# Optimization experiments

Measured on AMD Instinct MI355X. Metric: run time of the kernel, lower is better.

Reference implementation:

```python
import jax, jax.numpy as jnp
import numpy as np

# --- constants matching the torch module's default-camera / material / light setup ---
IMAGE_SIZE = 128
SCALE = 1.0
FOCAL = 12.0
R_MAT = jnp.array([[-1.0, 0.0, 0.0], [0.0, 1.0, 0.0], [0.0, 0.0, -1.0]], dtype=jnp.float32)
T_VEC = jnp.array([0.0, 0.0, 2.0 * SCALE], dtype=jnp.float32)
CAM_POS = jnp.array([0.0, 0.0, 2.0 * SCALE], dtype=jnp.float32)  # camera center in world coords
LIGHT_LOC = jnp.array([0.0, 1.0, 3.0], dtype=jnp.float32)
AMB_L, DIFF_L, SPEC_L = 0.5, 0.3, 0.2          # PointLights defaults
MAT_AMB, MAT_DIFF, MAT_SPEC = 1.0, 1.0, 0.6    # Materials(specular_color=0.6)
SHININESS = 10.0
TEXEL = jnp.array([142.0, 179.0, 247.0], dtype=jnp.float32) / 255.0  # uniform vertex color
BG = 1.0  # BlendParams background
EPS = 1e-8


def _normalize(v):
    return v / (jnp.linalg.norm(v, axis=-1, keepdims=True) + EPS)


def _render_one(verts, faces):
    """verts: [V,3] world space; faces: [F,3] int. Returns ([3,H,W] rgb*255, [1,H,W] alpha)."""
    H = W = IMAGE_SIZE
    # world -> view (PyTorch3D row-vector convention: x_view = x @ R + T)
    view = verts @ R_MAT + T_VEC              # [V,3]
    z = view[:, 2]                            # [V] view-space depth (>0 in front)
    ndc = FOCAL * view[:, :2] / z[:, None]    # [V,2] perspective projection to NDC
    tri = ndc[faces]                          # [F,3,2]
    tz = z[faces]                             # [F,3]

    # pixel centers in NDC (PyTorch3D: +x left, +y up)
    xs = 1.0 - (2.0 * jnp.arange(W) + 1.0) / W
    ys = 1.0 - (2.0 * jnp.arange(H) + 1.0) / H
    gy, gx = jnp.meshgrid(ys, xs, indexing='ij')
    px = gx.reshape(-1).astype(jnp.float32)   # [P]
    py = gy.reshape(-1).astype(jnp.float32)   # [P]

    v0, v1, v2 = tri[:, 0], tri[:, 1], tri[:, 2]   # [F,2]

    def edge(a, b):  # signed area cross(b-a, p-a) for all pixels -> [P,F]
        return ((b[:, 0] - a[:, 0])[None] * (py[:, None] - a[:, 1][None])
                - (b[:, 1] - a[:, 1])[None] * (px[:, None] - a[:, 0][None]))

    area = ((v1[:, 0] - v0[:, 0]) * (v2[:, 1] - v0[:, 1])
            - (v1[:, 1] - v0[:, 1]) * (v2[:, 0] - v0[:, 0]))   # [F]
    area_safe = jnp.where(jnp.abs(area) < EPS, EPS, area)
    b0 = edge(v1, v2) / area_safe             # [P,F]
    b1 = edge(v2, v0) / area_safe
    b2 = 1.0 - b0 - b1
    inside = (b0 >= 0) & (b1 >= 0) & (b2 >= 0) & (jnp.abs(area) > EPS)[None]

    # perspective-correct interpolated depth: z_pix = 1 / sum_i(b_i / z_i)
    S = b0 / tz[:, 0] + b1 / tz[:, 1] + b2 / tz[:, 2]
    depth = jnp.where(inside & (S > EPS), 1.0 / jnp.maximum(S, EPS), jnp.inf)
    fidx = jnp.argmin(depth, axis=1)          # [P] z-buffer winner (faces_per_pixel=1)
    hit = jnp.isfinite(jnp.min(depth, axis=1))

    # --- recompute barycentrics only for the winning face per pixel (cheap, [P]) ---
    f = faces[fidx]                           # [P,3]
    tv = ndc[f]                               # [P,3,2]
    tzp = z[f]                                # [P,3]
    a0, a1, a2 = tv[:, 0], tv[:, 1], tv[:, 2]

    def edge_p(a, b):
        return (b[:, 0] - a[:, 0]) * (py - a[:, 1]) - (b[:, 1] - a[:, 1]) * (px - a[:, 0])

    ar = (a1[:, 0] - a0[:, 0]) * (a2[:, 1] - a0[:, 1]) - (a1[:, 1] - a0[:, 1]) * (a2[:, 0] - a0[:, 0])
    ar = jnp.where(jnp.abs(ar) < EPS, EPS, ar)
    bb0 = edge_p(a1, a2) / ar
    bb1 = edge_p(a2, a0) / ar
    bb2 = 1.0 - bb0 - bb1
    w = jnp.stack([bb0 / tzp[:, 0], bb1 / tzp[:, 1], bb2 / tzp[:, 2]], axis=-1)
    pc = w / (jnp.sum(w, axis=-1, keepdims=True) + EPS)   # [P,3] perspective-correct barycentrics

    # --- vertex normals (world space) ---
    fv = verts[faces]                         # [F,3,3]
    fn = jnp.cross(fv[:, 1] - fv[:, 0], fv[:, 2] - fv[:, 0])  # [F,3]
    vn = (jnp.zeros_like(verts)
          .at[faces[:, 0]].add(fn)
          .at[faces[:, 1]].add(fn)
          .at[faces[:, 2]].add(fn))
    vn = _normalize(vn)

    # --- interpolate position/normal, Phong shade ---
    pos = jnp.einsum('pk,pkd->pd', pc, verts[f])   # [P,3]
    nrm = _normalize(jnp.einsum('pk,pkd->pd', pc, vn[f]))
    l = _normalize(LIGHT_LOC - pos)
    vdir = _normalize(CAM_POS - pos)
    ndl = jax.nn.relu(jnp.sum(nrm * l, axis=-1))          # [P]
    refl = 2.0 * jnp.sum(nrm * l, axis=-1, keepdims=True) * nrm - l
    spec_cos = jax.nn.relu(jnp.sum(refl * vdir, axis=-1))
    ambient = AMB_L * MAT_AMB
    diffuse = DIFF_L * MAT_DIFF * ndl
    specular = SPEC_L * MAT_SPEC * spec_cos ** SHININESS
    color = TEXEL[None] * (ambient + diffuse[:, None]) + specular[:, None]

    rgb = jnp.where(hit[:, None], color, BG)              # hard blend with white bg
    alpha = hit.astype(verts.dtype)
    img = rgb.reshape(H, W, 3).transpose(2, 0, 1) * 255.0  # [3,H,W]
    a = alpha.reshape(1, H, W)
    return img, a


def setup_inputs() -> dict:
    key = jax.random.key(0)
    k1, k2 = jax.random.split(key)
    B, V, F = 2, 1300, 2500
    vertices = jax.random.normal(k1, (B, V, 3), dtype=jnp.float32) * 0.05  # head-scale mesh near origin
    faces = jax.random.randint(k2, (F, 3), 0, V, dtype=jnp.int32)
    return {"vertices": vertices, "faces": faces}


def reference(vertices, faces):
    # ori_size == image_size, so the area-interpolation in the torch module is the identity.
    images, alphas = jax.lax.map(lambda v: _render_one(v, faces), vertices)
    return images, alphas
```

## Files before the change

kernel.cpp:

```cpp
#include <hip/hip_runtime.h>
#include <math.h>

#pragma clang fp contract(off)

#define IMG_H 128
#define IMG_W 128
#define HW (IMG_H * IMG_W)
#define NB 2
#define NV 1300
#define NF 2500
#define EPSF 1e-8f
#define NCHUNK 32
#define CHUNK ((NF + NCHUNK - 1) / NCHUNK)
#define NBLK (64 * NB * NCHUNK)

#define OFF_VN 41600
#define OFF_FACE 72800
#define OFF_DBUF 392800

#define DINIT 0x7F800000FFFFFFFFull

__global__ __launch_bounds__(256) void k_init(const float* __restrict__ verts,
                                              float4* __restrict__ vert,
                                              float* __restrict__ vn) {
    int i = blockIdx.x * 256 + threadIdx.x;
    if (i < NB * NV * 3) vn[i] = 0.0f;
    if (i < NB * NV) {
        float vx = verts[i * 3 + 0];
        float vy = verts[i * 3 + 1];
        float vz = verts[i * 3 + 2];
        float viewx = -vx;
        float viewy = vy;
        float z = 2.0f - vz;
        float ndcx = (12.0f * viewx) / z;
        float ndcy = (12.0f * viewy) / z;
        vert[i] = make_float4(ndcx, ndcy, z, 0.0f);
    }
}

__global__ __launch_bounds__(256) void k_face(const float* __restrict__ verts,
                                              const int* __restrict__ faces,
                                              const float4* __restrict__ vert,
                                              float* __restrict__ vn,
                                              float4* __restrict__ face) {
    int i = blockIdx.x * 256 + threadIdx.x;
    if (i >= NB * NF) return;
    int b = i / NF;
    int f = i - b * NF;
    int i0 = faces[f * 3 + 0];
    int i1 = faces[f * 3 + 1];
    int i2 = faces[f * 3 + 2];
    float4 p0 = vert[b * NV + i0];
    float4 p1 = vert[b * NV + i1];
    float4 p2 = vert[b * NV + i2];
    float t1 = (p1.x - p0.x) * (p2.y - p0.y);
    float t2 = (p1.y - p0.y) * (p2.x - p0.x);
    float area = t1 - t2;
    float aabs = fabsf(area);
    float area_safe = (aabs < EPSF) ? EPSF : area;
    bool valid = aabs > EPSF;
    float minx, maxx, miny, maxy;
    if (valid) {
        minx = fminf(p0.x, fminf(p1.x, p2.x)) - 1e-3f;
        maxx = fmaxf(p0.x, fmaxf(p1.x, p2.x)) + 1e-3f;
        miny = fminf(p0.y, fminf(p1.y, p2.y)) - 1e-3f;
        maxy = fmaxf(p0.y, fmaxf(p1.y, p2.y)) + 1e-3f;
    } else {
        minx = 1e30f; maxx = -1e30f; miny = 1e30f; maxy = -1e30f;
    }
    int o = (b * NF + f) * 4;
    face[o + 0] = make_float4(p2.x - p1.x, p2.y - p1.y, p1.x, p1.y);
    face[o + 1] = make_float4(p0.x - p2.x, p0.y - p2.y, p2.x, p2.y);
    face[o + 2] = make_float4(area_safe, p0.z, p1.z, p2.z);
    face[o + 3] = make_float4(minx, maxx, miny, maxy);

    const float* wv = verts + (size_t)b * NV * 3;
    float ax = wv[i1 * 3 + 0] - wv[i0 * 3 + 0];
    float ay = wv[i1 * 3 + 1] - wv[i0 * 3 + 1];
    float az = wv[i1 * 3 + 2] - wv[i0 * 3 + 2];
    float bx = wv[i2 * 3 + 0] - wv[i0 * 3 + 0];
    float by = wv[i2 * 3 + 1] - wv[i0 * 3 + 1];
    float bz = wv[i2 * 3 + 2] - wv[i0 * 3 + 2];
    float fnx = ay * bz - az * by;
    float fny = az * bx - ax * bz;
    float fnz = ax * by - ay * bx;
    float* vnb = vn + (size_t)b * NV * 3;
    atomicAdd(&vnb[i0 * 3 + 0], fnx);
    atomicAdd(&vnb[i0 * 3 + 1], fny);
    atomicAdd(&vnb[i0 * 3 + 2], fnz);
    atomicAdd(&vnb[i1 * 3 + 0], fnx);
    atomicAdd(&vnb[i1 * 3 + 1], fny);
    atomicAdd(&vnb[i1 * 3 + 2], fnz);
    atomicAdd(&vnb[i2 * 3 + 0], fnx);
    atomicAdd(&vnb[i2 * 3 + 1], fny);
    atomicAdd(&vnb[i2 * 3 + 2], fnz);
}

__global__ __launch_bounds__(256) void k_raster(const float4* __restrict__ face,
                                                unsigned long long* __restrict__ dbuf) {
    __shared__ float4 sface[CHUNK * 4];
    __shared__ int sidx[CHUNK];
    __shared__ int swbase[4];
    __shared__ int scnt;

    int idx = (blockIdx.x * 1213) & (NBLK - 1);
    int chunk = idx & (NCHUNK - 1);
    int tmp = idx >> 5;
    int b = tmp & 1;
    int tile = tmp >> 1;
    int f0 = chunk * CHUNK;
    int nf = NF - f0; if (nf > CHUNK) nf = CHUNK;

    int r0 = (tile >> 3) * 16;
    int c0 = (tile & 7) * 16;
    float txmax = 1.0f - (2.0f * (float)c0 + 1.0f) / 128.0f;
    float txmin = 1.0f - (2.0f * (float)(c0 + 15) + 1.0f) / 128.0f;
    float tymax = 1.0f - (2.0f * (float)r0 + 1.0f) / 128.0f;
    float tymin = 1.0f - (2.0f * (float)(r0 + 15) + 1.0f) / 128.0f;

    const float4* fb = face + (size_t)b * NF * 4;
    int t = threadIdx.x;
    int wid = t >> 6, lid = t & 63;
    bool pass = false;
    float4 bb;
    if (t < nf) {
        bb = fb[(f0 + t) * 4 + 3];
        pass = (bb.y >= txmin) && (bb.x <= txmax) && (bb.w >= tymin) && (bb.z <= tymax);
    }
    unsigned long long m = __ballot(pass);
    if (lid == 0) swbase[wid] = __popcll(m);
    __syncthreads();
    if (t == 0) {
        int acc = 0;
        for (int i2 = 0; i2 < 4; ++i2) { int cc = swbase[i2]; swbase[i2] = acc; acc += cc; }
        scnt = acc;
    }
    __syncthreads();
    if (pass) {
        int pos = swbase[wid] + __popcll(m & ((1ull << lid) - 1ull));
        sface[pos * 4 + 0] = fb[(f0 + t) * 4 + 0];
        sface[pos * 4 + 1] = fb[(f0 + t) * 4 + 1];
        sface[pos * 4 + 2] = fb[(f0 + t) * 4 + 2];
        sface[pos * 4 + 3] = bb;
        sidx[pos] = f0 + t;
    }
    __syncthreads();
    int cnt = scnt;

    int r = r0 + ((wid >> 1) * 8) + (lid >> 3);
    int c = c0 + ((wid & 1) * 8) + (lid & 7);
    int p = r * IMG_W + c;
    float px = 1.0f - (2.0f * (float)c + 1.0f) / 128.0f;
    float py = 1.0f - (2.0f * (float)r + 1.0f) / 128.0f;

    unsigned long long best = DINIT;
    for (int j = 0; j < cnt; ++j) {
        float4 fbb = sface[j * 4 + 3];
        if (px >= fbb.x && px <= fbb.y && py >= fbb.z && py <= fbb.w) {
            float4 E0 = sface[j * 4 + 0];
            float4 E1 = sface[j * 4 + 1];
            float4 FD = sface[j * 4 + 2];
            float u1 = E0.x * (py - E0.w);
            float u2 = E0.y * (px - E0.z);
            float e0 = u1 - u2;
            float u3 = E1.x * (py - E1.w);
            float u4 = E1.y * (px - E1.z);
            float e1 = u3 - u4;
            float as = FD.x;
            bool ok = (as > 0.0f) ? (e0 >= 0.0f && e1 >= 0.0f)
                                  : (e0 <= 0.0f && e1 <= 0.0f);
            if (ok) {
                float b0 = e0 / as;
                float b1 = e1 / as;
                float b2 = (1.0f - b0) - b1;
                if (b2 >= 0.0f) {
                    float S = ((b0 / FD.y) + (b1 / FD.z)) + (b2 / FD.w);
                    if (S > EPSF) {
                        float depth = 1.0f / fmaxf(S, EPSF);
                        unsigned long long pk =
                            ((unsigned long long)__float_as_uint(depth) << 32) |
                            (unsigned)sidx[j];
                        if (pk < best) best = pk;
                    }
                }
            }
        }
    }
    dbuf[((size_t)chunk * NB + b) * HW + p] = best;
}

__global__ __launch_bounds__(256) void k_shade(const float* __restrict__ verts,
                                               const int* __restrict__ faces,
                                               const float4* __restrict__ vert,
                                               const float* __restrict__ vn,
                                               const unsigned long long* __restrict__ dbuf,
                                               float* __restrict__ out) {
    int i = blockIdx.x * 256 + threadIdx.x;
    int b = i >> 14;
    int p = i & (HW - 1);
    unsigned long long pk = DINIT;
    for (int k = 0; k < NCHUNK; ++k) {
        unsigned long long v = dbuf[((size_t)k * NB + b) * HW + p];
        if (v < pk) pk = v;
    }
    unsigned dbits = (unsigned)(pk >> 32);
    bool hit = dbits < 0x7F800000u;
    float cr = 255.0f, cg = 255.0f, cb = 255.0f, alpha = 0.0f;
    if (hit) {
        alpha = 1.0f;
        int f = (int)(unsigned)(pk & 0xFFFFFFFFull);
        int row = p >> 7;
        int col = p & 127;
        float px = 1.0f - (2.0f * (float)col + 1.0f) / 128.0f;
        float py = 1.0f - (2.0f * (float)row + 1.0f) / 128.0f;
        int i0 = faces[f * 3 + 0];
        int i1 = faces[f * 3 + 1];
        int i2 = faces[f * 3 + 2];
        float4 a0 = vert[b * NV + i0];
        float4 a1 = vert[b * NV + i1];
        float4 a2 = vert[b * NV + i2];
        float t1 = (a1.x - a0.x) * (a2.y - a0.y);
        float t2 = (a1.y - a0.y) * (a2.x - a0.x);
        float ar = t1 - t2;
        ar = (fabsf(ar) < EPSF) ? EPSF : ar;
        float u1 = (a2.x - a1.x) * (py - a1.y);
        float u2 = (a2.y - a1.y) * (px - a1.x);
        float bb0 = (u1 - u2) / ar;
        float u3 = (a0.x - a2.x) * (py - a2.y);
        float u4 = (a0.y - a2.y) * (px - a2.x);
        float bb1 = (u3 - u4) / ar;
        float bb2 = (1.0f - bb0) - bb1;
        float w0 = bb0 / a0.z;
        float w1 = bb1 / a1.z;
        float w2 = bb2 / a2.z;
        float denom = ((w0 + w1) + w2) + EPSF;
        float pc0 = w0 / denom;
        float pc1 = w1 / denom;
        float pc2 = w2 / denom;

        const float* wv = verts + (size_t)b * NV * 3;
        float v0x = wv[i0 * 3 + 0], v0y = wv[i0 * 3 + 1], v0z = wv[i0 * 3 + 2];
        float v1x = wv[i1 * 3 + 0], v1y = wv[i1 * 3 + 1], v1z = wv[i1 * 3 + 2];
        float v2x = wv[i2 * 3 + 0], v2y = wv[i2 * 3 + 1], v2z = wv[i2 * 3 + 2];
        float posx = (pc0 * v0x + pc1 * v1x) + pc2 * v2x;
        float posy = (pc0 * v0y + pc1 * v1y) + pc2 * v2y;
        float posz = (pc0 * v0z + pc1 * v1z) + pc2 * v2z;

        const float* vnb = vn + (size_t)b * NV * 3;
        float n0x = vnb[i0 * 3 + 0], n0y = vnb[i0 * 3 + 1], n0z = vnb[i0 * 3 + 2];
        float n1x = vnb[i1 * 3 + 0], n1y = vnb[i1 * 3 + 1], n1z = vnb[i1 * 3 + 2];
        float n2x = vnb[i2 * 3 + 0], n2y = vnb[i2 * 3 + 1], n2z = vnb[i2 * 3 + 2];
        float in0 = 1.0f / (sqrtf(n0x * n0x + n0y * n0y + n0z * n0z) + EPSF);
        float in1 = 1.0f / (sqrtf(n1x * n1x + n1y * n1y + n1z * n1z) + EPSF);
        float in2 = 1.0f / (sqrtf(n2x * n2x + n2y * n2y + n2z * n2z) + EPSF);
        n0x *= in0; n0y *= in0; n0z *= in0;
        n1x *= in1; n1y *= in1; n1z *= in1;
        n2x *= in2; n2y *= in2; n2z *= in2;
        float nx = (pc0 * n0x + pc1 * n1x) + pc2 * n2x;
        float ny = (pc0 * n0y + pc1 * n1y) + pc2 * n2y;
        float nz = (pc0 * n0z + pc1 * n1z) + pc2 * n2z;
        float inn = 1.0f / (sqrtf(nx * nx + ny * ny + nz * nz) + EPSF);
        nx *= inn; ny *= inn; nz *= inn;

        float lx = 0.0f - posx, ly = 1.0f - posy, lz = 3.0f - posz;
        float iln = 1.0f / (sqrtf(lx * lx + ly * ly + lz * lz) + EPSF);
        lx *= iln; ly *= iln; lz *= iln;
        float vx = 0.0f - posx, vy = 0.0f - posy, vz = 2.0f - posz;
        float ivn = 1.0f / (sqrtf(vx * vx + vy * vy + vz * vz) + EPSF);
        vx *= ivn; vy *= ivn; vz *= ivn;

        float ndl = nx * lx + ny * ly + nz * lz;
        float ndlr = fmaxf(ndl, 0.0f);
        float rx = 2.0f * ndl * nx - lx;
        float ry = 2.0f * ndl * ny - ly;
        float rz = 2.0f * ndl * nz - lz;
        float sc = fmaxf(rx * vx + ry * vy + rz * vz, 0.0f);
        float spec = 0.2f * 0.6f * powf(sc, 10.0f);
        float shade = 0.5f * 1.0f + 0.3f * 1.0f * ndlr;
        cr = ((142.0f / 255.0f) * shade + spec) * 255.0f;
        cg = ((179.0f / 255.0f) * shade + spec) * 255.0f;
        cb = ((247.0f / 255.0f) * shade + spec) * 255.0f;
    }
    float* img = out + (size_t)b * 3 * HW;
    img[0 * HW + p] = cr;
    img[1 * HW + p] = cg;
    img[2 * HW + p] = cb;
    out[(size_t)NB * 3 * HW + (size_t)b * HW + p] = alpha;
}

extern "C" void kernel_launch(void* const* d_in, const int* in_sizes, int n_in,
                              void* d_out, int out_size, void* d_ws, size_t ws_size,
                              hipStream_t stream) {
    const float* verts = (const float*)d_in[0];
    const int* faces = (const int*)d_in[1];
    char* ws = (char*)d_ws;
    float4* vert = (float4*)(ws + 0);
    float* vn = (float*)(ws + OFF_VN);
    float4* face = (float4*)(ws + OFF_FACE);
    unsigned long long* dbuf = (unsigned long long*)(ws + OFF_DBUF);
    float* out = (float*)d_out;

    k_init<<<(NB * NV * 3 + 255) / 256, 256, 0, stream>>>(verts, vert, vn);
    k_face<<<(NB * NF + 255) / 256, 256, 0, stream>>>(verts, faces, vert, vn, face);
    k_raster<<<NBLK, 256, 0, stream>>>(face, dbuf);
    k_shade<<<(NB * HW) / 256, 256, 0, stream>>>(verts, faces, vert, vn, dbuf, out);
}
```

Baseline: 111.3 us.

## Fold vertex projection into face and shade kernels, shrink raster tiles to 128 threads

Removes the k_init kernel: the face and shade kernels now project vertices themselves, and the normal buffer is cleared with hipMemsetAsync. This saves a launch and the intermediate vertex buffer. The raster kernel switches to 128-thread blocks covering 8x16 tiles, which doubles the block count and drops one barrier from the compaction step. It also drops the blockIdx scrambling. The cost is some redundant projection arithmetic and less face reuse per block.

```diff
diff --git a/kernel.cpp b/kernel.cpp
--- a/kernel.cpp
+++ b/kernel.cpp
@@ -12,35 +12,16 @@
 #define EPSF 1e-8f
 #define NCHUNK 32
 #define CHUNK ((NF + NCHUNK - 1) / NCHUNK)
-#define NBLK (64 * NB * NCHUNK)
-
-#define OFF_VN 41600
-#define OFF_FACE 72800
-#define OFF_DBUF 392800
+#define NREG 128
+#define NBLK (NREG * NB * NCHUNK)
+
+#define OFF_FACE 31232
+#define OFF_DBUF 351488
 
 #define DINIT 0x7F800000FFFFFFFFull
-
-__global__ __launch_bounds__(256) void k_init(const float* __restrict__ verts,
-                                              float4* __restrict__ vert,
-                                              float* __restrict__ vn) {
-    int i = blockIdx.x * 256 + threadIdx.x;
-    if (i < NB * NV * 3) vn[i] = 0.0f;
-    if (i < NB * NV) {
-        float vx = verts[i * 3 + 0];
-        float vy = verts[i * 3 + 1];
-        float vz = verts[i * 3 + 2];
-        float viewx = -vx;
-        float viewy = vy;
-        float z = 2.0f - vz;
-        float ndcx = (12.0f * viewx) / z;
-        float ndcy = (12.0f * viewy) / z;
-        vert[i] = make_float4(ndcx, ndcy, z, 0.0f);
-    }
-}
 
 __global__ __launch_bounds__(256) void k_face(const float* __restrict__ verts,
                                               const int* __restrict__ faces,
-                                              const float4* __restrict__ vert,
                                               float* __restrict__ vn,
                                               float4* __restrict__ face) {
     int i = blockIdx.x * 256 + threadIdx.x;
@@ -50,37 +31,38 @@
     int i0 = faces[f * 3 + 0];
     int i1 = faces[f * 3 + 1];
     int i2 = faces[f * 3 + 2];
-    float4 p0 = vert[b * NV + i0];
-    float4 p1 = vert[b * NV + i1];
-    float4 p2 = vert[b * NV + i2];
-    float t1 = (p1.x - p0.x) * (p2.y - p0.y);
-    float t2 = (p1.y - p0.y) * (p2.x - p0.x);
+    const float* wv = verts + (size_t)b * NV * 3;
+    float v0x = wv[i0 * 3 + 0], v0y = wv[i0 * 3 + 1], v0z = wv[i0 * 3 + 2];
+    float v1x = wv[i1 * 3 + 0], v1y = wv[i1 * 3 + 1], v1z = wv[i1 * 3 + 2];
+    float v2x = wv[i2 * 3 + 0], v2y = wv[i2 * 3 + 1], v2z = wv[i2 * 3 + 2];
+    float z0 = 2.0f - v0z, z1 = 2.0f - v1z, z2 = 2.0f - v2z;
+    float p0x = (12.0f * (-v0x)) / z0, p0y = (12.0f * v0y) / z0;
+    float p1x = (12.0f * (-v1x)) / z1, p1y = (12.0f * v1y) / z1;
+    float p2x = (12.0f * (-v2x)) / z2, p2y = (12.0f * v2y) / z2;
+
+    float t1 = (p1x - p0x) * (p2y - p0y);
+    float t2 = (p1y - p0y) * (p2x - p0x);
     float area = t1 - t2;
     float aabs = fabsf(area);
     float area_safe = (aabs < EPSF) ? EPSF : area;
     bool valid = aabs > EPSF;
     float minx, maxx, miny, maxy;
     if (valid) {
-        minx = fminf(p0.x, fminf(p1.x, p2.x)) - 1e-3f;
-        maxx = fmaxf(p0.x, fmaxf(p1.x, p2.x)) + 1e-3f;
-        miny = fminf(p0.y, fminf(p1.y, p2.y)) - 1e-3f;
-        maxy = fmaxf(p0.y, fmaxf(p1.y, p2.y)) + 1e-3f;
+        minx = fminf(p0x, fminf(p1x, p2x)) - 1e-3f;
+        maxx = fmaxf(p0x, fmaxf(p1x, p2x)) + 1e-3f;
+        miny = fminf(p0y, fminf(p1y, p2y)) - 1e-3f;
+        maxy = fmaxf(p0y, fmaxf(p1y, p2y)) + 1e-3f;
     } else {
         minx = 1e30f; maxx = -1e30f; miny = 1e30f; maxy = -1e30f;
     }
     int o = (b * NF + f) * 4;
-    face[o + 0] = make_float4(p2.x - p1.x, p2.y - p1.y, p1.x, p1.y);
-    face[o + 1] = make_float4(p0.x - p2.x, p0.y - p2.y, p2.x, p2.y);
-    face[o + 2] = make_float4(area_safe, p0.z, p1.z, p2.z);
+    face[o + 0] = make_float4(p2x - p1x, p2y - p1y, p1x, p1y);
+    face[o + 1] = make_float4(p0x - p2x, p0y - p2y, p2x, p2y);
+    face[o + 2] = make_float4(area_safe, z0, z1, z2);
     face[o + 3] = make_float4(minx, maxx, miny, maxy);
 
-    const float* wv = verts + (size_t)b * NV * 3;
-    float ax = wv[i1 * 3 + 0] - wv[i0 * 3 + 0];
-    float ay = wv[i1 * 3 + 1] - wv[i0 * 3 + 1];
-    float az = wv[i1 * 3 + 2] - wv[i0 * 3 + 2];
-    float bx = wv[i2 * 3 + 0] - wv[i0 * 3 + 0];
-    float by = wv[i2 * 3 + 1] - wv[i0 * 3 + 1];
-    float bz = wv[i2 * 3 + 2] - wv[i0 * 3 + 2];
+    float ax = v1x - v0x, ay = v1y - v0y, az = v1z - v0z;
+    float bx = v2x - v0x, by = v2y - v0y, bz = v2z - v0z;
     float fnx = ay * bz - az * by;
     float fny = az * bx - ax * bz;
     float fnz = ax * by - ay * bx;
@@ -96,27 +78,27 @@
     atomicAdd(&vnb[i2 * 3 + 2], fnz);
 }
 
-__global__ __launch_bounds__(256) void k_raster(const float4* __restrict__ face,
+__global__ __launch_bounds__(128) void k_raster(const float4* __restrict__ face,
                                                 unsigned long long* __restrict__ dbuf) {
     __shared__ float4 sface[CHUNK * 4];
     __shared__ int sidx[CHUNK];
-    __shared__ int swbase[4];
+    __shared__ int swbase[2];
     __shared__ int scnt;
 
-    int idx = (blockIdx.x * 1213) & (NBLK - 1);
-    int chunk = idx & (NCHUNK - 1);
-    int tmp = idx >> 5;
+    int bx = blockIdx.x;
+    int chunk = bx & (NCHUNK - 1);
+    int tmp = bx >> 5;
     int b = tmp & 1;
-    int tile = tmp >> 1;
+    int reg = tmp >> 1;
+    int r0 = (reg >> 3) * 8;
+    int c0 = (reg & 7) * 16;
     int f0 = chunk * CHUNK;
     int nf = NF - f0; if (nf > CHUNK) nf = CHUNK;
 
-    int r0 = (tile >> 3) * 16;
-    int c0 = (tile & 7) * 16;
     float txmax = 1.0f - (2.0f * (float)c0 + 1.0f) / 128.0f;
     float txmin = 1.0f - (2.0f * (float)(c0 + 15) + 1.0f) / 128.0f;
     float tymax = 1.0f - (2.0f * (float)r0 + 1.0f) / 128.0f;
-    float tymin = 1.0f - (2.0f * (float)(r0 + 15) + 1.0f) / 128.0f;
+    float tymin = 1.0f - (2.0f * (float)(r0 + 7) + 1.0f) / 128.0f;
 
     const float4* fb = face + (size_t)b * NF * 4;
     int t = threadIdx.x;
@@ -130,25 +112,21 @@
     unsigned long long m = __ballot(pass);
     if (lid == 0) swbase[wid] = __popcll(m);
     __syncthreads();
-    if (t == 0) {
-        int acc = 0;
-        for (int i2 = 0; i2 < 4; ++i2) { int cc = swbase[i2]; swbase[i2] = acc; acc += cc; }
-        scnt = acc;
-    }
-    __syncthreads();
+    int base0 = swbase[0];
     if (pass) {
-        int pos = swbase[wid] + __popcll(m & ((1ull << lid) - 1ull));
+        int pos = (wid ? base0 : 0) + __popcll(m & ((1ull << lid) - 1ull));
         sface[pos * 4 + 0] = fb[(f0 + t) * 4 + 0];
         sface[pos * 4 + 1] = fb[(f0 + t) * 4 + 1];
         sface[pos * 4 + 2] = fb[(f0 + t) * 4 + 2];
         sface[pos * 4 + 3] = bb;
         sidx[pos] = f0 + t;
     }
+    if (t == 0) scnt = base0 + swbase[1];
     __syncthreads();
     int cnt = scnt;
 
-    int r = r0 + ((wid >> 1) * 8) + (lid >> 3);
-    int c = c0 + ((wid & 1) * 8) + (lid & 7);
+    int r = r0 + (lid >> 3);
+    int c = c0 + wid * 8 + (lid & 7);
     int p = r * IMG_W + c;
     float px = 1.0f - (2.0f * (float)c + 1.0f) / 128.0f;
     float py = 1.0f - (2.0f * (float)r + 1.0f) / 128.0f;
@@ -191,7 +169,6 @@
 
 __global__ __launch_bounds__(256) void k_shade(const float* __restrict__ verts,
                                                const int* __restrict__ faces,
-                                               const float4* __restrict__ vert,
                                                const float* __restrict__ vn,
                                                const unsigned long long* __restrict__ dbuf,
                                                float* __restrict__ out) {
@@ -216,32 +193,34 @@
         int i0 = faces[f * 3 + 0];
         int i1 = faces[f * 3 + 1];
         int i2 = faces[f * 3 + 2];
-        float4 a0 = vert[b * NV + i0];
-        float4 a1 = vert[b * NV + i1];
-        float4 a2 = vert[b * NV + i2];
-        float t1 = (a1.x - a0.x) * (a2.y - a0.y);
-        float t2 = (a1.y - a0.y) * (a2.x - a0.x);
+        const float* wv = verts + (size_t)b * NV * 3;
+        float v0x = wv[i0 * 3 + 0], v0y = wv[i0 * 3 + 1], v0z = wv[i0 * 3 + 2];
+        float v1x = wv[i1 * 3 + 0], v1y = wv[i1 * 3 + 1], v1z = wv[i1 * 3 + 2];
+        float v2x = wv[i2 * 3 + 0], v2y = wv[i2 * 3 + 1], v2z = wv[i2 * 3 + 2];
+        float z0 = 2.0f - v0z, z1 = 2.0f - v1z, z2 = 2.0f - v2z;
+        float a0x = (12.0f * (-v0x)) / z0, a0y = (12.0f * v0y) / z0;
+        float a1x = (12.0f * (-v1x)) / z1, a1y = (12.0f * v1y) / z1;
+        float a2x = (12.0f * (-v2x)) / z2, a2y = (12.0f * v2y) / z2;
+
+        float t1 = (a1x - a0x) * (a2y - a0y);
+        float t2 = (a1y - a0y) * (a2x - a0x);
         float ar = t1 - t2;
         ar = (fabsf(ar) < EPSF) ? EPSF : ar;
-        float u1 = (a2.x - a1.x) * (py - a1.y);
-        float u2 = (a2.y - a1.y) * (px - a1.x);
+        float u1 = (a2x - a1x) * (py - a1y);
+        float u2 = (a2y - a1y) * (px - a1x);
         float bb0 = (u1 - u2) / ar;
-        float u3 = (a0.x - a2.x) * (py - a2.y);
-        float u4 = (a0.y - a2.y) * (px - a2.x);
+        float u3 = (a0x - a2x) * (py - a2y);
+        float u4 = (a0y - a2y) * (px - a2x);
         float bb1 = (u3 - u4) / ar;
         float bb2 = (1.0f - bb0) - bb1;
-        float w0 = bb0 / a0.z;
-        float w1 = bb1 / a1.z;
-        float w2 = bb2 / a2.z;
+        float w0 = bb0 / z0;
+        float w1 = bb1 / z1;
+        float w2 = bb2 / z2;
         float denom = ((w0 + w1) + w2) + EPSF;
         float pc0 = w0 / denom;
         float pc1 = w1 / denom;
         float pc2 = w2 / denom;
 
-        const float* wv = verts + (size_t)b * NV * 3;
-        float v0x = wv[i0 * 3 + 0], v0y = wv[i0 * 3 + 1], v0z = wv[i0 * 3 + 2];
-        float v1x = wv[i1 * 3 + 0], v1y = wv[i1 * 3 + 1], v1z = wv[i1 * 3 + 2];
-        float v2x = wv[i2 * 3 + 0], v2y = wv[i2 * 3 + 1], v2z = wv[i2 * 3 + 2];
         float posx = (pc0 * v0x + pc1 * v1x) + pc2 * v2x;
         float posy = (pc0 * v0y + pc1 * v1y) + pc2 * v2y;
         float posz = (pc0 * v0z + pc1 * v1z) + pc2 * v2z;
@@ -294,14 +273,13 @@
     const float* verts = (const float*)d_in[0];
     const int* faces = (const int*)d_in[1];
     char* ws = (char*)d_ws;
-    float4* vert = (float4*)(ws + 0);
-    float* vn = (float*)(ws + OFF_VN);
+    float* vn = (float*)(ws + 0);
     float4* face = (float4*)(ws + OFF_FACE);
     unsigned long long* dbuf = (unsigned long long*)(ws + OFF_DBUF);
     float* out = (float*)d_out;
 
-    k_init<<<(NB * NV * 3 + 255) / 256, 256, 0, stream>>>(verts, vert, vn);
-    k_face<<<(NB * NF + 255) / 256, 256, 0, stream>>>(verts, faces, vert, vn, face);
-    k_raster<<<NBLK, 256, 0, stream>>>(face, dbuf);
-    k_shade<<<(NB * HW) / 256, 256, 0, stream>>>(verts, faces, vert, vn, dbuf, out);
-}
+    hipMemsetAsync(vn, 0, NB * NV * 3 * sizeof(float), stream);
+    k_face<<<(NB * NF + 255) / 256, 256, 0, stream>>>(verts, faces, vn, face);
+    k_raster<<<NBLK, 128, 0, stream>>>(face, dbuf);
+    k_shade<<<(NB * HW) / 256, 256, 0, stream>>>(verts, faces, vn, dbuf, out);
+}
```

New measurement: 103.5 us. 1.07x faster.
